# Optimization experiments

Hardware: AMD Instinct MI355X
Metric: run time of the kernel (lower is better)

The kernel has to match this reference:

```python
import jax, jax.numpy as jnp
import numpy as np

B, S, H, E = 2, 2048, 16, 64
INV_SCALE = 8.0  # sqrt(head_dim); forward divides scores by this


def setup_inputs() -> dict:
    key = jax.random.key(0)
    ks = jax.random.split(key, 10)
    return {
        "query": jax.random.normal(ks[0], (B, S, H, E), dtype=jnp.float32),
        "key": jax.random.normal(ks[1], (B, S, H, E), dtype=jnp.float32),
        "value": jax.random.normal(ks[2], (B, S, H, E), dtype=jnp.float32),
        "attn_mask": jax.random.randint(ks[3], (B, S), 0, 2, dtype=jnp.int32),
        "Wq": jax.random.normal(ks[4], (E, E), dtype=jnp.float32) / np.sqrt(E),
        "bq": jax.random.normal(ks[5], (E,), dtype=jnp.float32) * 0.02,
        "Wk": jax.random.normal(ks[6], (E, E), dtype=jnp.float32) / np.sqrt(E),
        "bk": jax.random.normal(ks[7], (E,), dtype=jnp.float32) * 0.02,
        "Wv": jax.random.normal(ks[8], (E, E), dtype=jnp.float32) / np.sqrt(E),
        "bv": jax.random.normal(ks[9], (E,), dtype=jnp.float32) * 0.02,
    }


def reference(query, key, value, attn_mask, Wq, bq, Wk, bk, Wv, bv):
    # Linear projections over the last (embed) dim; torch Linear: x @ W.T + b
    q = jnp.einsum('bshe,fe->bhsf', query, Wq) + bq  # [B,H,S,E] (permute 0,2,1,3 fused)
    k = jnp.einsum('bshe,fe->bhsf', key, Wk) + bk
    v = jnp.einsum('bshe,fe->bhsf', value, Wv) + bv
    scores = jnp.einsum('bhqe,bhke->bhqk', q, k) / INV_SCALE  # [B,H,S,S]
    # mask: positions where attn_mask == 0 get -inf, broadcast over (1,1,k_len)
    masked = attn_mask[:, None, None, :] == 0  # [B,1,1,S]
    scores = jnp.where(masked, -jnp.inf, scores)
    attn = jax.nn.softmax(scores, axis=-1)
    out = jnp.einsum('bhqk,bhke->bqhe', attn, v)  # permute back to [B,S,H,E]
    return out
```

## Files before the change

### kernel.cpp

```cpp
#include <hip/hip_runtime.h>


#define BATCH 2
#define SEQ   2048
#define NH    16
#define DE    64
#define LDP   72
#define LDOF  68
#define NKT   (SEQ / 64)
#define LOG2E 1.44269504088896340736f
#define CSHIFT 16.0f

using bf16x8   = __attribute__((ext_vector_type(8))) __bf16;
using bf16x4   = __attribute__((ext_vector_type(4))) __bf16;
using bf16x2   = __attribute__((ext_vector_type(2))) __bf16;
using floatx2  = __attribute__((ext_vector_type(2))) float;
using floatx4  = __attribute__((ext_vector_type(4))) float;
using floatx16 = __attribute__((ext_vector_type(16))) float;
using ushortx4 = __attribute__((ext_vector_type(4))) unsigned short;
using ushortx8 = __attribute__((ext_vector_type(8))) unsigned short;
using uintx4   = __attribute__((ext_vector_type(4))) unsigned int;

__device__ __forceinline__ ushortx4 cvt4(floatx4 f) {
    bf16x4 h = __builtin_convertvector(f, bf16x4);
    return __builtin_bit_cast(ushortx4, h);
}

__device__ __forceinline__ unsigned int pkbf16(float a, float b) {
    floatx2 f = {a, b};
    return __builtin_bit_cast(unsigned int, __builtin_convertvector(f, bf16x2));
}

__device__ __forceinline__ void pl32swap(unsigned int& x, unsigned int& y) {
    __asm__ volatile("v_permlane32_swap_b32 %0, %1" : "+v"(x), "+v"(y));
}

__device__ __forceinline__ void glds16(const unsigned short* g, unsigned short* l) {
    __builtin_amdgcn_global_load_lds(
        (const __attribute__((address_space(1))) unsigned int*)g,
        (__attribute__((address_space(3))) unsigned int*)l, 16, 0, 0);
}

__global__ __launch_bounds__(256) void proj_kernel(
    const float* __restrict__ xq, const float* __restrict__ xk, const float* __restrict__ xv,
    const float* __restrict__ Wq, const float* __restrict__ bq,
    const float* __restrict__ Wk, const float* __restrict__ bk,
    const float* __restrict__ Wv, const float* __restrict__ bv,
    unsigned short* __restrict__ qb, unsigned short* __restrict__ kb,
    unsigned short* __restrict__ vtb)
{
    __shared__ __align__(16) unsigned short Xb[64 * LDP];
    __shared__ __align__(16) unsigned short Wb[64 * LDP];
    __shared__ __align__(16) unsigned short Ob[64 * LDP];
    __shared__ float blds[64];

    const int t  = threadIdx.x;
    const int p  = blockIdx.x >> 10;
    const int bh = (blockIdx.x >> 5) & 31;
    const int st = blockIdx.x & 31;
    const int s0 = st * 64;
    const int b  = bh >> 4, h = bh & 15;
    const int lane = t & 63, w = t >> 6, quad = lane >> 4, l16 = lane & 15;

    const float* x    = (p == 0) ? xq : (p == 1) ? xk : xv;
    const float* W    = (p == 0) ? Wq : (p == 1) ? Wk : Wv;
    const float* bias = (p == 0) ? bq : (p == 1) ? bk : bv;

    #pragma unroll
    for (int i = 0; i < 4; ++i) {
        int idx = i * 1024 + t * 4;
        int row = idx >> 6, col = idx & 63;
        floatx4 xv4 = *(const floatx4*)(x + (((size_t)(b * SEQ + s0 + row) * NH + h) * DE + col));
        *(ushortx4*)&Xb[row * LDP + col] = cvt4(xv4);
        floatx4 wv4 = *(const floatx4*)(W + row * 64 + col);
        *(ushortx4*)&Wb[row * LDP + col] = cvt4(wv4);
    }
    if (t < 64) blds[t] = bias[t];
    __syncthreads();

    if (p < 2) {
        bf16x8 a0 = *(const bf16x8*)&Wb[(w * 16 + l16) * LDP + quad * 8];
        bf16x8 a1 = *(const bf16x8*)&Wb[(w * 16 + l16) * LDP + 32 + quad * 8];
        floatx4 bf4 = *(const floatx4*)&blds[w * 16 + quad * 4];
        const float scale = (p == 0) ? 0.125f * LOG2E : 1.0f;
        #pragma unroll
        for (int nb = 0; nb < 4; ++nb) {
            bf16x8 b0 = *(const bf16x8*)&Xb[(nb * 16 + l16) * LDP + quad * 8];
            bf16x8 b1 = *(const bf16x8*)&Xb[(nb * 16 + l16) * LDP + 32 + quad * 8];
            floatx4 c = {0.f, 0.f, 0.f, 0.f};
            c = __builtin_amdgcn_mfma_f32_16x16x32_bf16(a0, b0, c, 0, 0, 0);
            c = __builtin_amdgcn_mfma_f32_16x16x32_bf16(a1, b1, c, 0, 0, 0);
            floatx4 v;
            v[0] = (c[0] + bf4[0]) * scale; v[1] = (c[1] + bf4[1]) * scale;
            v[2] = (c[2] + bf4[2]) * scale; v[3] = (c[3] + bf4[3]) * scale;
            *(ushortx4*)&Ob[(nb * 16 + l16) * LDP + w * 16 + quad * 4] = cvt4(v);
        }
    } else {
        bf16x8 a0 = *(const bf16x8*)&Xb[(w * 16 + l16) * LDP + quad * 8];
        bf16x8 a1 = *(const bf16x8*)&Xb[(w * 16 + l16) * LDP + 32 + quad * 8];
        #pragma unroll
        for (int nb = 0; nb < 4; ++nb) {
            bf16x8 b0 = *(const bf16x8*)&Wb[(nb * 16 + l16) * LDP + quad * 8];
            bf16x8 b1 = *(const bf16x8*)&Wb[(nb * 16 + l16) * LDP + 32 + quad * 8];
            floatx4 c = {0.f, 0.f, 0.f, 0.f};
            c = __builtin_amdgcn_mfma_f32_16x16x32_bf16(a0, b0, c, 0, 0, 0);
            c = __builtin_amdgcn_mfma_f32_16x16x32_bf16(a1, b1, c, 0, 0, 0);
            float bw = blds[nb * 16 + l16];
            floatx4 v;
            v[0] = c[0] + bw; v[1] = c[1] + bw; v[2] = c[2] + bw; v[3] = c[3] + bw;
            *(ushortx4*)&Ob[(nb * 16 + l16) * LDP + w * 16 + quad * 4] = cvt4(v);
        }
    }
    __syncthreads();

    #pragma unroll
    for (int j = 0; j < 2; ++j) {
        int idx = j * 256 + t;
        int row = idx >> 3, c = idx & 7;
        int cp  = (c ^ (row & 7)) * 8;
        ushortx8 v = *(const ushortx8*)&Ob[row * LDP + c * 8];
        if (p < 2) {
            unsigned short* dst = (p == 0) ? qb : kb;
            *(ushortx8*)(dst + ((size_t)bh * SEQ + s0 + row) * DE + cp) = v;
        } else {
            *(ushortx8*)(vtb + ((size_t)bh * DE + row) * SEQ + s0 + cp) = v;
        }
    }
}

__global__ __launch_bounds__(512, 4) void attn_kernel(
    const unsigned short* __restrict__ qb, const unsigned short* __restrict__ kb,
    const unsigned short* __restrict__ vtb, const int* __restrict__ mask,
    float* __restrict__ out)
{
    __shared__ __align__(16) char smem[16384 + 16384 + 16384 + 512];
    unsigned short* Kl = (unsigned short*)smem;
    unsigned short* Vl = (unsigned short*)(smem + 16384);
    unsigned short* Pq = (unsigned short*)(smem + 32768);
    float*          Ml = (float*)(smem + 49152);
    float*          Ol = (float*)smem;
    float*          Ll = (float*)(smem + 34816);

    const int t  = threadIdx.x;
    const int qt = blockIdx.x, bh = blockIdx.y;
    const int b  = bh >> 4, h = bh & 15;
    const int q0 = qt * 128;
    const int lane = t & 63, w = t >> 6;
    const int hi = lane >> 5, l31 = lane & 31;
    const int qw = w & 3, kblk = w >> 2;
    const int sw7 = l31 & 7;

    const unsigned short* kbase = kb + (size_t)bh * SEQ * DE;
    const unsigned short* vbase = vtb + (size_t)bh * DE * SEQ;
    const unsigned short* qsrc  = qb + ((size_t)bh * SEQ + q0) * DE;
    const int* mrow = mask + b * SEQ;

    glds16(qsrc + (w * 16) * DE + lane * 8,      Pq + (w * 16) * 64);
    glds16(qsrc + (w * 16 + 8) * DE + lane * 8,  Pq + (w * 16 + 8) * 64);
    glds16(kbase + (size_t)(w * 8) * DE + lane * 8, Kl + w * 512);
    glds16(vbase + (size_t)(w * 8 + (lane >> 3)) * SEQ + (lane & 7) * 8, Vl + w * 512);
    if (t < 64) Ml[t] = mrow[t] ? -CSHIFT : -1e30f;
    int mreg = (t < 64) ? mrow[64 + t] : 0;
    __syncthreads();

    bf16x8 qf[4];
    #pragma unroll
    for (int ks = 0; ks < 4; ++ks)
        qf[ks] = *(const bf16x8*)&Pq[(qw * 32 + l31) * 64 + (((ks * 2 + hi) ^ sw7) * 8)];

    floatx16 o0, o1;
    #pragma unroll
    for (int i = 0; i < 16; ++i) { o0[i] = 0.f; o1[i] = 0.f; }
    float lp = 0.f;

    for (int kt = 0; kt < NKT; ++kt) {
        const int cur = kt & 1, nxt = cur ^ 1;
        const unsigned short* Kc = Kl + cur * 4096;
        const unsigned short* Vc = Vl + cur * 4096;
        const float*          Mc = Ml + cur * 64;

        if (kt + 1 < NKT) {
            const int k1 = (kt + 1) * 64;
            glds16(kbase + (size_t)(k1 + w * 8) * DE + lane * 8, Kl + nxt * 4096 + w * 512);
            glds16(vbase + (size_t)(w * 8 + (lane >> 3)) * SEQ + k1 + (lane & 7) * 8,
                   Vl + nxt * 4096 + w * 512);
            if (t < 64) Ml[nxt * 64 + t] = mreg ? -CSHIFT : -1e30f;
            mreg = (t < 64 && kt + 2 < NKT) ? mrow[(kt + 2) * 64 + t] : 0;
        }

        floatx16 sc;
        #pragma unroll
        for (int g = 0; g < 4; ++g) {
            floatx4 mb = *(const floatx4*)&Mc[kblk * 32 + g * 8 + hi * 4];
            sc[4 * g + 0] = mb[0]; sc[4 * g + 1] = mb[1];
            sc[4 * g + 2] = mb[2]; sc[4 * g + 3] = mb[3];
        }
        #pragma unroll
        for (int ks = 0; ks < 4; ++ks) {
            bf16x8 kf = *(const bf16x8*)&Kc[(kblk * 32 + l31) * 64 + (((ks * 2 + hi) ^ sw7) * 8)];
            sc = __builtin_amdgcn_mfma_f32_32x32x16_bf16(kf, qf[ks], sc, 0, 0, 0);
        }

        #pragma unroll
        for (int r = 0; r < 16; ++r)
            sc[r] = __builtin_amdgcn_exp2f(sc[r]);
        {
            float a0 = sc[0] + sc[1],   a1 = sc[2] + sc[3];
            float a2 = sc[4] + sc[5],   a3 = sc[6] + sc[7];
            float a4 = sc[8] + sc[9],   a5 = sc[10] + sc[11];
            float a6 = sc[12] + sc[13], a7 = sc[14] + sc[15];
            lp += ((a0 + a1) + (a2 + a3)) + ((a4 + a5) + (a6 + a7));
        }

        unsigned int wd0 = pkbf16(sc[0], sc[1]),   wd1 = pkbf16(sc[2], sc[3]);
        unsigned int wd2 = pkbf16(sc[4], sc[5]),   wd3 = pkbf16(sc[6], sc[7]);
        unsigned int wd4 = pkbf16(sc[8], sc[9]),   wd5 = pkbf16(sc[10], sc[11]);
        unsigned int wd6 = pkbf16(sc[12], sc[13]), wd7 = pkbf16(sc[14], sc[15]);
        pl32swap(wd0, wd2); pl32swap(wd1, wd3);
        pl32swap(wd4, wd6); pl32swap(wd5, wd7);
        uintx4 f0v = {wd0, wd1, wd2, wd3};
        uintx4 f1v = {wd4, wd5, wd6, wd7};
        bf16x8 pf0 = __builtin_bit_cast(bf16x8, f0v);
        bf16x8 pf1 = __builtin_bit_cast(bf16x8, f1v);

        #pragma unroll
        for (int s = 0; s < 2; ++s) {
            const bf16x8 pf = s ? pf1 : pf0;
            const int cc = ((kblk * 4 + s * 2 + hi) ^ sw7) * 8;
            bf16x8 v0 = *(const bf16x8*)&Vc[l31 * 64 + cc];
            bf16x8 v1 = *(const bf16x8*)&Vc[(32 + l31) * 64 + cc];
            o0 = __builtin_amdgcn_mfma_f32_32x32x16_bf16(v0, pf, o0, 0, 0, 0);
            o1 = __builtin_amdgcn_mfma_f32_32x32x16_bf16(v1, pf, o1, 0, 0, 0);
        }

        __syncthreads();
    }

    const int qrow = qw * 32 + l31;
    Ll[qrow * 4 + kblk * 2 + hi] = lp;
    if (kblk == 1) {
        #pragma unroll
        for (int g = 0; g < 4; ++g) {
            floatx4 t0 = {o0[4*g+0], o0[4*g+1], o0[4*g+2], o0[4*g+3]};
            *(floatx4*)&Ol[qrow * LDOF + g * 8 + hi * 4] = t0;
            floatx4 t1 = {o1[4*g+0], o1[4*g+1], o1[4*g+2], o1[4*g+3]};
            *(floatx4*)&Ol[qrow * LDOF + 32 + g * 8 + hi * 4] = t1;
        }
    }
    __syncthreads();
    if (kblk == 0) {
        floatx4 lv = *(const floatx4*)&Ll[qrow * 4];
        float invl = __builtin_amdgcn_rcpf(lv[0] + lv[1] + lv[2] + lv[3]);
        #pragma unroll
        for (int g = 0; g < 4; ++g) {
            floatx4 t0 = *(floatx4*)&Ol[qrow * LDOF + g * 8 + hi * 4];
            t0[0] = (t0[0] + o0[4*g+0]) * invl; t0[1] = (t0[1] + o0[4*g+1]) * invl;
            t0[2] = (t0[2] + o0[4*g+2]) * invl; t0[3] = (t0[3] + o0[4*g+3]) * invl;
            *(floatx4*)&Ol[qrow * LDOF + g * 8 + hi * 4] = t0;
            floatx4 t1 = *(floatx4*)&Ol[qrow * LDOF + 32 + g * 8 + hi * 4];
            t1[0] = (t1[0] + o1[4*g+0]) * invl; t1[1] = (t1[1] + o1[4*g+1]) * invl;
            t1[2] = (t1[2] + o1[4*g+2]) * invl; t1[3] = (t1[3] + o1[4*g+3]) * invl;
            *(floatx4*)&Ol[qrow * LDOF + 32 + g * 8 + hi * 4] = t1;
        }
    }
    __syncthreads();
    {
        const int quad = lane >> 4, l16 = lane & 15;
        #pragma unroll
        for (int pass = 0; pass < 4; ++pass) {
            int rl  = w * 16 + pass * 4 + quad;
            int col = l16 * 4;
            floatx4 tv = *(const floatx4*)&Ol[rl * LDOF + col];
            *(floatx4*)(out + (((size_t)b * SEQ + q0 + rl) * NH + h) * DE + col) = tv;
        }
    }
}

extern "C" void kernel_launch(void* const* d_in, const int* in_sizes, int n_in,
                              void* d_out, int out_size, void* d_ws, size_t ws_size,
                              hipStream_t stream) {
    const float* query = (const float*)d_in[0];
    const float* key   = (const float*)d_in[1];
    const float* value = (const float*)d_in[2];
    const int*   mask  = (const int*)d_in[3];
    const float* Wq = (const float*)d_in[4];
    const float* bq = (const float*)d_in[5];
    const float* Wk = (const float*)d_in[6];
    const float* bk = (const float*)d_in[7];
    const float* Wv = (const float*)d_in[8];
    const float* bv = (const float*)d_in[9];

    const size_t tensor_elems = (size_t)BATCH * NH * SEQ * DE;
    unsigned short* qb  = (unsigned short*)d_ws;
    unsigned short* kb  = qb + tensor_elems;
    unsigned short* vtb = kb + tensor_elems;

    proj_kernel<<<dim3(3 * BATCH * NH * (SEQ / 64)), 256, 0, stream>>>(
        query, key, value, Wq, bq, Wk, bk, Wv, bv, qb, kb, vtb);
    attn_kernel<<<dim3(SEQ / 128, BATCH * NH), 512, 0, stream>>>(
        qb, kb, vtb, mask, (float*)d_out);
}
```

Baseline: 150.9 us.

## Use MFMA row-sum, split barriers with explicit waitcnt, and raise MFMA priority

```diff
diff --git a/kernel.cpp b/kernel.cpp
--- a/kernel.cpp
+++ b/kernel.cpp
@@ -159,8 +159,8 @@
     glds16(qsrc + (w * 16 + 8) * DE + lane * 8,  Pq + (w * 16 + 8) * 64);
     glds16(kbase + (size_t)(w * 8) * DE + lane * 8, Kl + w * 512);
     glds16(vbase + (size_t)(w * 8 + (lane >> 3)) * SEQ + (lane & 7) * 8, Vl + w * 512);
-    if (t < 64) Ml[t] = mrow[t] ? -CSHIFT : -1e30f;
-    int mreg = (t < 64) ? mrow[64 + t] : 0;
+    if (w == 0) Ml[lane] = mrow[lane] ? -CSHIFT : -1e30f;
+    int mreg = mrow[64 + lane];
     __syncthreads();
 
     bf16x8 qf[4];
@@ -168,10 +168,13 @@
     for (int ks = 0; ks < 4; ++ks)
         qf[ks] = *(const bf16x8*)&Pq[(qw * 32 + l31) * 64 + (((ks * 2 + hi) ^ sw7) * 8)];
 
-    floatx16 o0, o1;
-    #pragma unroll
-    for (int i = 0; i < 16; ++i) { o0[i] = 0.f; o1[i] = 0.f; }
-    float lp = 0.f;
+    bf16x8 onesf;
+    #pragma unroll
+    for (int i = 0; i < 8; ++i) onesf[i] = (__bf16)1.0f;
+
+    floatx16 o0, o1, acc_l;
+    #pragma unroll
+    for (int i = 0; i < 16; ++i) { o0[i] = 0.f; o1[i] = 0.f; acc_l[i] = 0.f; }
 
     for (int kt = 0; kt < NKT; ++kt) {
         const int cur = kt & 1, nxt = cur ^ 1;
@@ -179,14 +182,23 @@
         const unsigned short* Vc = Vl + cur * 4096;
         const float*          Mc = Ml + cur * 64;
 
+        __builtin_amdgcn_sched_barrier(0);
+        __builtin_amdgcn_s_barrier();
+
         if (kt + 1 < NKT) {
             const int k1 = (kt + 1) * 64;
             glds16(kbase + (size_t)(k1 + w * 8) * DE + lane * 8, Kl + nxt * 4096 + w * 512);
             glds16(vbase + (size_t)(w * 8 + (lane >> 3)) * SEQ + k1 + (lane & 7) * 8,
                    Vl + nxt * 4096 + w * 512);
-            if (t < 64) Ml[nxt * 64 + t] = mreg ? -CSHIFT : -1e30f;
-            mreg = (t < 64 && kt + 2 < NKT) ? mrow[(kt + 2) * 64 + t] : 0;
-        }
+            if (w == 0) Ml[nxt * 64 + lane] = mreg ? -CSHIFT : -1e30f;
+            const int midx = (kt + 2 < NKT) ? ((kt + 2) * 64 + lane) : lane;
+            mreg = mrow[midx];
+            __asm__ volatile("s_waitcnt vmcnt(3) lgkmcnt(0)" ::: "memory");
+        } else {
+            __asm__ volatile("s_waitcnt vmcnt(0) lgkmcnt(0)" ::: "memory");
+        }
+        __builtin_amdgcn_s_barrier();
+        __builtin_amdgcn_sched_barrier(0);
 
         floatx16 sc;
         #pragma unroll
@@ -195,22 +207,17 @@
             sc[4 * g + 0] = mb[0]; sc[4 * g + 1] = mb[1];
             sc[4 * g + 2] = mb[2]; sc[4 * g + 3] = mb[3];
         }
+        __builtin_amdgcn_s_setprio(1);
         #pragma unroll
         for (int ks = 0; ks < 4; ++ks) {
             bf16x8 kf = *(const bf16x8*)&Kc[(kblk * 32 + l31) * 64 + (((ks * 2 + hi) ^ sw7) * 8)];
             sc = __builtin_amdgcn_mfma_f32_32x32x16_bf16(kf, qf[ks], sc, 0, 0, 0);
         }
+        __builtin_amdgcn_s_setprio(0);
 
         #pragma unroll
         for (int r = 0; r < 16; ++r)
             sc[r] = __builtin_amdgcn_exp2f(sc[r]);
-        {
-            float a0 = sc[0] + sc[1],   a1 = sc[2] + sc[3];
-            float a2 = sc[4] + sc[5],   a3 = sc[6] + sc[7];
-            float a4 = sc[8] + sc[9],   a5 = sc[10] + sc[11];
-            float a6 = sc[12] + sc[13], a7 = sc[14] + sc[15];
-            lp += ((a0 + a1) + (a2 + a3)) + ((a4 + a5) + (a6 + a7));
-        }
 
         unsigned int wd0 = pkbf16(sc[0], sc[1]),   wd1 = pkbf16(sc[2], sc[3]);
         unsigned int wd2 = pkbf16(sc[4], sc[5]),   wd3 = pkbf16(sc[6], sc[7]);
@@ -223,6 +230,7 @@
         bf16x8 pf0 = __builtin_bit_cast(bf16x8, f0v);
         bf16x8 pf1 = __builtin_bit_cast(bf16x8, f1v);
 
+        __builtin_amdgcn_s_setprio(1);
         #pragma unroll
         for (int s = 0; s < 2; ++s) {
             const bf16x8 pf = s ? pf1 : pf0;
@@ -232,12 +240,14 @@
             o0 = __builtin_amdgcn_mfma_f32_32x32x16_bf16(v0, pf, o0, 0, 0, 0);
             o1 = __builtin_amdgcn_mfma_f32_32x32x16_bf16(v1, pf, o1, 0, 0, 0);
         }
-
-        __syncthreads();
-    }
-
+        acc_l = __builtin_amdgcn_mfma_f32_32x32x16_bf16(onesf, pf0, acc_l, 0, 0, 0);
+        acc_l = __builtin_amdgcn_mfma_f32_32x32x16_bf16(onesf, pf1, acc_l, 0, 0, 0);
+        __builtin_amdgcn_s_setprio(0);
+    }
+
+    __syncthreads();
     const int qrow = qw * 32 + l31;
-    Ll[qrow * 4 + kblk * 2 + hi] = lp;
+    if (hi == 0) Ll[qrow * 2 + kblk] = acc_l[0];
     if (kblk == 1) {
         #pragma unroll
         for (int g = 0; g < 4; ++g) {
@@ -249,8 +259,7 @@
     }
     __syncthreads();
     if (kblk == 0) {
-        floatx4 lv = *(const floatx4*)&Ll[qrow * 4];
-        float invl = __builtin_amdgcn_rcpf(lv[0] + lv[1] + lv[2] + lv[3]);
+        float invl = __builtin_amdgcn_rcpf(Ll[qrow * 2] + Ll[qrow * 2 + 1]);
         #pragma unroll
         for (int g = 0; g < 4; ++g) {
             floatx4 t0 = *(floatx4*)&Ol[qrow * LDOF + g * 8 + hi * 4];
```

Result: no change. 150.5 us (-0.3%).

## Retile projection kernel to read contiguous 8-head x 16-seq input chunks

Applied to the files above, without the earlier changes.

```diff
diff --git a/kernel.cpp b/kernel.cpp
--- a/kernel.cpp
+++ b/kernel.cpp
@@ -5,7 +5,6 @@
 #define SEQ   2048
 #define NH    16
 #define DE    64
-#define LDP   72
 #define LDOF  68
 #define NKT   (SEQ / 64)
 #define LOG2E 1.44269504088896340736f
@@ -49,17 +48,18 @@
     unsigned short* __restrict__ qb, unsigned short* __restrict__ kb,
     unsigned short* __restrict__ vtb)
 {
-    __shared__ __align__(16) unsigned short Xb[64 * LDP];
-    __shared__ __align__(16) unsigned short Wb[64 * LDP];
-    __shared__ __align__(16) unsigned short Ob[64 * LDP];
+    __shared__ __align__(16) unsigned short Wb[64 * 72];
+    __shared__ __align__(16) unsigned short Xb[8 * 1160];
+    __shared__ __align__(16) unsigned short Ob[12288];
     __shared__ float blds[64];
 
     const int t  = threadIdx.x;
-    const int p  = blockIdx.x >> 10;
-    const int bh = (blockIdx.x >> 5) & 31;
-    const int st = blockIdx.x & 31;
-    const int s0 = st * 64;
-    const int b  = bh >> 4, h = bh & 15;
+    const int bi = blockIdx.x;
+    const int hh = bi & 1;
+    const int st = (bi >> 1) & 127;
+    const int b  = (bi >> 8) & 1;
+    const int p  = bi >> 9;
+    const int h0 = hh * 8;
     const int lane = t & 63, w = t >> 6, quad = lane >> 4, l16 = lane & 15;
 
     const float* x    = (p == 0) ? xq : (p == 1) ? xk : xv;
@@ -67,63 +67,76 @@
     const float* bias = (p == 0) ? bq : (p == 1) ? bk : bv;
 
     #pragma unroll
+    for (int i = 0; i < 8; ++i) {
+        int idx = i * 256 + t;
+        int s = idx >> 7, rem = idx & 127, h = rem >> 4, e4 = (rem & 15) * 4;
+        floatx4 xv4 = *(const floatx4*)(x + ((size_t)(b * SEQ + st * 16 + s) * NH + h0 + h) * DE + e4);
+        *(ushortx4*)&Xb[h * 1160 + s * 72 + e4] = cvt4(xv4);
+    }
+    #pragma unroll
     for (int i = 0; i < 4; ++i) {
-        int idx = i * 1024 + t * 4;
-        int row = idx >> 6, col = idx & 63;
-        floatx4 xv4 = *(const floatx4*)(x + (((size_t)(b * SEQ + s0 + row) * NH + h) * DE + col));
-        *(ushortx4*)&Xb[row * LDP + col] = cvt4(xv4);
-        floatx4 wv4 = *(const floatx4*)(W + row * 64 + col);
-        *(ushortx4*)&Wb[row * LDP + col] = cvt4(wv4);
+        int idx = i * 256 + t;
+        int row = idx >> 4, c4 = (idx & 15) * 4;
+        floatx4 wv4 = *(const floatx4*)(W + row * 64 + c4);
+        *(ushortx4*)&Wb[row * 72 + c4] = cvt4(wv4);
     }
     if (t < 64) blds[t] = bias[t];
     __syncthreads();
 
     if (p < 2) {
-        bf16x8 a0 = *(const bf16x8*)&Wb[(w * 16 + l16) * LDP + quad * 8];
-        bf16x8 a1 = *(const bf16x8*)&Wb[(w * 16 + l16) * LDP + 32 + quad * 8];
+        bf16x8 a0 = *(const bf16x8*)&Wb[(w * 16 + l16) * 72 + quad * 8];
+        bf16x8 a1 = *(const bf16x8*)&Wb[(w * 16 + l16) * 72 + 32 + quad * 8];
         floatx4 bf4 = *(const floatx4*)&blds[w * 16 + quad * 4];
         const float scale = (p == 0) ? 0.125f * LOG2E : 1.0f;
         #pragma unroll
-        for (int nb = 0; nb < 4; ++nb) {
-            bf16x8 b0 = *(const bf16x8*)&Xb[(nb * 16 + l16) * LDP + quad * 8];
-            bf16x8 b1 = *(const bf16x8*)&Xb[(nb * 16 + l16) * LDP + 32 + quad * 8];
+        for (int h = 0; h < 8; ++h) {
+            bf16x8 b0 = *(const bf16x8*)&Xb[h * 1160 + l16 * 72 + quad * 8];
+            bf16x8 b1 = *(const bf16x8*)&Xb[h * 1160 + l16 * 72 + 32 + quad * 8];
             floatx4 c = {0.f, 0.f, 0.f, 0.f};
             c = __builtin_amdgcn_mfma_f32_16x16x32_bf16(a0, b0, c, 0, 0, 0);
             c = __builtin_amdgcn_mfma_f32_16x16x32_bf16(a1, b1, c, 0, 0, 0);
             floatx4 v;
             v[0] = (c[0] + bf4[0]) * scale; v[1] = (c[1] + bf4[1]) * scale;
             v[2] = (c[2] + bf4[2]) * scale; v[3] = (c[3] + bf4[3]) * scale;
-            *(ushortx4*)&Ob[(nb * 16 + l16) * LDP + w * 16 + quad * 4] = cvt4(v);
+            *(ushortx4*)&Ob[h * 1160 + l16 * 72 + w * 16 + quad * 4] = cvt4(v);
         }
     } else {
-        bf16x8 a0 = *(const bf16x8*)&Xb[(w * 16 + l16) * LDP + quad * 8];
-        bf16x8 a1 = *(const bf16x8*)&Xb[(w * 16 + l16) * LDP + 32 + quad * 8];
-        #pragma unroll
-        for (int nb = 0; nb < 4; ++nb) {
-            bf16x8 b0 = *(const bf16x8*)&Wb[(nb * 16 + l16) * LDP + quad * 8];
-            bf16x8 b1 = *(const bf16x8*)&Wb[(nb * 16 + l16) * LDP + 32 + quad * 8];
+        bf16x8 b0 = *(const bf16x8*)&Wb[(w * 16 + l16) * 72 + quad * 8];
+        bf16x8 b1 = *(const bf16x8*)&Wb[(w * 16 + l16) * 72 + 32 + quad * 8];
+        const float bw = blds[w * 16 + l16];
+        #pragma unroll
+        for (int h = 0; h < 8; ++h) {
+            bf16x8 a0 = *(const bf16x8*)&Xb[h * 1160 + l16 * 72 + quad * 8];
+            bf16x8 a1 = *(const bf16x8*)&Xb[h * 1160 + l16 * 72 + 32 + quad * 8];
             floatx4 c = {0.f, 0.f, 0.f, 0.f};
             c = __builtin_amdgcn_mfma_f32_16x16x32_bf16(a0, b0, c, 0, 0, 0);
             c = __builtin_amdgcn_mfma_f32_16x16x32_bf16(a1, b1, c, 0, 0, 0);
-            float bw = blds[nb * 16 + l16];
             floatx4 v;
             v[0] = c[0] + bw; v[1] = c[1] + bw; v[2] = c[2] + bw; v[3] = c[3] + bw;
-            *(ushortx4*)&Ob[(nb * 16 + l16) * LDP + w * 16 + quad * 4] = cvt4(v);
-        }
-    }
-    __syncthreads();
-
-    #pragma unroll
-    for (int j = 0; j < 2; ++j) {
-        int idx = j * 256 + t;
-        int row = idx >> 3, c = idx & 7;
-        int cp  = (c ^ (row & 7)) * 8;
-        ushortx8 v = *(const ushortx8*)&Ob[row * LDP + c * 8];
-        if (p < 2) {
-            unsigned short* dst = (p == 0) ? qb : kb;
-            *(ushortx8*)(dst + ((size_t)bh * SEQ + s0 + row) * DE + cp) = v;
-        } else {
-            *(ushortx8*)(vtb + ((size_t)bh * DE + row) * SEQ + s0 + cp) = v;
+            *(ushortx4*)&Ob[h * 1536 + (w * 16 + l16) * 24 + quad * 4] = cvt4(v);
+        }
+    }
+    __syncthreads();
+
+    if (p < 2) {
+        unsigned short* dst = (p == 0) ? qb : kb;
+        #pragma unroll
+        for (int i = 0; i < 4; ++i) {
+            int idx = i * 256 + t;
+            int c = idx & 7, s = (idx >> 3) & 15, h = idx >> 7;
+            ushortx8 v = *(const ushortx8*)&Ob[h * 1160 + s * 72 + c * 8];
+            *(ushortx8*)(dst + ((size_t)(b * 16 + h0 + h) * SEQ + st * 16 + s) * 64
+                         + ((c ^ (s & 7)) * 8)) = v;
+        }
+    } else {
+        #pragma unroll
+        for (int i = 0; i < 4; ++i) {
+            int idx = i * 256 + t;
+            int cl = idx & 1, e = (idx >> 1) & 63, h = idx >> 7;
+            ushortx8 v = *(const ushortx8*)&Ob[h * 1536 + e * 24 + cl * 8];
+            int c = (st & 3) * 2 + cl;
+            *(ushortx8*)(vtb + ((size_t)(b * 16 + h0 + h) * 64 + e) * SEQ
+                         + (st >> 2) * 64 + ((c ^ (e & 7)) * 8)) = v;
         }
     }
 }
@@ -295,7 +308,7 @@
     unsigned short* kb  = qb + tensor_elems;
     unsigned short* vtb = kb + tensor_elems;
 
-    proj_kernel<<<dim3(3 * BATCH * NH * (SEQ / 64)), 256, 0, stream>>>(
+    proj_kernel<<<dim3(3 * BATCH * 128 * 2), 256, 0, stream>>>(
         query, key, value, Wq, bq, Wk, bk, Wv, bv, qb, kb, vtb);
     attn_kernel<<<dim3(SEQ / 128, BATCH * NH), 512, 0, stream>>>(
         qb, kb, vtb, mask, (float*)d_out);
```

Result: no change. 152.2 us (+0.9%).
